# Kernel tuning notes

Measured on AMD Instinct MI355X. Metric: run time of the kernel, lower is better.

## Reference

```python
import jax, jax.numpy as jnp
import numpy as np

WS = 7; SHIFT = 3; HEADS = 4; DIM = 192; C2 = 2 * DIM; HD = C2 // HEADS
H = W = 60
PAD = (WS - H % WS) % WS          # 3
HP = H + PAD; WP = W + PAD        # 63
NW = (HP // WS) * (WP // WS)      # 81 windows
N = WS * WS                       # 49 tokens per window
MLP_H = int(4.0 * C2)             # 1536


def _rel_pos_index():
    coords = np.stack(np.meshgrid(np.arange(WS), np.arange(WS), indexing='ij'))
    cf = coords.reshape(2, -1)
    rel = (cf[:, :, None] - cf[:, None, :]).transpose(1, 2, 0)
    rel[:, :, 0] += WS - 1
    rel[:, :, 1] += WS - 1
    rel[:, :, 0] *= 2 * WS - 1
    return rel.sum(-1)  # (N, N) into table of size (2*WS-1)^2


def _attn_mask():
    img = np.zeros((HP, WP))
    cnt = 0
    for hs in (slice(0, -WS), slice(-WS, -SHIFT), slice(-SHIFT, None)):
        for ws_ in (slice(0, -WS), slice(-WS, -SHIFT), slice(-SHIFT, None)):
            img[hs, ws_] = cnt; cnt += 1
    mw = img.reshape(HP // WS, WS, WP // WS, WS).transpose(0, 2, 1, 3).reshape(-1, N)
    diff = mw[:, None, :] - mw[:, :, None]
    return np.where(diff != 0, -100.0, 0.0).astype(np.float32)  # (NW, N, N)

REL_IDX = jnp.asarray(_rel_pos_index().reshape(-1))
ATTN_MASK = jnp.asarray(_attn_mask())


def layernorm(x, w, b, eps=1e-5):
    mu = jnp.mean(x, axis=-1, keepdims=True)
    var = jnp.var(x, axis=-1, keepdims=True)
    return (x - mu) * jax.lax.rsqrt(var + eps) * w + b


def setup_inputs() -> dict:
    key = jax.random.key(0)
    ks = jax.random.split(key, 16)
    s = 0.02
    return {
        'x': jax.random.normal(ks[0], (8, DIM, H, W), jnp.float32),
        'g': jax.random.normal(ks[1], (8, DIM, H, W), jnp.float32),
        'norm_w': jnp.ones((C2,), jnp.float32),
        'norm_b': jnp.zeros((C2,), jnp.float32),
        'n1_w': jnp.ones((C2,), jnp.float32),
        'n1_b': jnp.zeros((C2,), jnp.float32),
        'qkv_w': jax.random.normal(ks[2], (3 * C2, C2), jnp.float32) * s,
        'qkv_b': jnp.zeros((3 * C2,), jnp.float32),
        'proj_w': jax.random.normal(ks[3], (C2, C2), jnp.float32) * s,
        'proj_b': jnp.zeros((C2,), jnp.float32),
        'rpb': jax.random.normal(ks[4], ((2 * WS - 1) ** 2, HEADS), jnp.float32) * s,
        'n2_w': jnp.ones((C2,), jnp.float32),
        'n2_b': jnp.zeros((C2,), jnp.float32),
        'fc1_w': jax.random.normal(ks[5], (MLP_H, C2), jnp.float32) * s,
        'fc1_b': jnp.zeros((MLP_H,), jnp.float32),
        'fc2_w': jax.random.normal(ks[6], (C2, MLP_H), jnp.float32) * s,
        'fc2_b': jnp.zeros((C2,), jnp.float32),
        'conv_w': jax.random.normal(ks[7], (DIM, C2, 3, 3), jnp.float32) * s,
        'conv_b': jnp.zeros((DIM,), jnp.float32),
    }


def reference(x, g, norm_w, norm_b, n1_w, n1_b, qkv_w, qkv_b, proj_w, proj_b,
              rpb, n2_w, n2_b, fc1_w, fc1_b, fc2_w, fc2_b, conv_w, conv_b):
    B = x.shape[0]
    # concat + NCHW -> NHWC + pad to window multiple
    comb = jnp.concatenate([x, g], axis=1).transpose(0, 2, 3, 1)   # (B,H,W,2C)
    comb = jnp.pad(comb, ((0, 0), (0, PAD), (0, PAD), (0, 0)))     # (B,HP,WP,2C)
    z = layernorm(comb, norm_w, norm_b)
    # ---- Swin block ----
    shortcut = z
    zn = layernorm(z, n1_w, n1_b)
    zn = jnp.roll(zn, shift=(-SHIFT, -SHIFT), axis=(1, 2))
    # window partition -> (B*NW, N, 2C)
    w = zn.reshape(B, HP // WS, WS, WP // WS, WS, C2).transpose(0, 1, 3, 2, 4, 5)
    w = w.reshape(B * NW, N, C2)
    qkv = (w @ qkv_w.T + qkv_b).reshape(B * NW, N, 3, HEADS, HD).transpose(2, 0, 3, 1, 4)
    q, k, v = qkv[0], qkv[1], qkv[2]                               # (B*NW,H,N,HD)
    attn = jnp.einsum('bhnd,bhmd->bhnm', q, k) * (HD ** -0.5)
    bias = rpb[REL_IDX].reshape(N, N, HEADS).transpose(2, 0, 1)    # (H,N,N)
    attn = attn + bias[None]
    attn = attn.reshape(B, NW, HEADS, N, N) + ATTN_MASK[None, :, None]
    attn = jax.nn.softmax(attn.reshape(B * NW, HEADS, N, N), axis=-1)
    out = jnp.einsum('bhnm,bhmd->bhnd', attn, v).transpose(0, 2, 1, 3).reshape(B * NW, N, C2)
    out = out @ proj_w.T + proj_b
    # window reverse + unshift
    out = out.reshape(B, HP // WS, WP // WS, WS, WS, C2).transpose(0, 1, 3, 2, 4, 5)
    out = out.reshape(B, HP, WP, C2)
    out = jnp.roll(out, shift=(SHIFT, SHIFT), axis=(1, 2))
    z = shortcut + out
    h = layernorm(z, n2_w, n2_b)
    h = jax.nn.gelu(h @ fc1_w.T + fc1_b, approximate=False)
    z = z + (h @ fc2_w.T + fc2_b)
    # crop, NHWC -> NCHW, 3x3 reduce conv, residual
    z = z[:, :H, :W, :].transpose(0, 3, 1, 2)                      # (B,2C,H,W)
    red = jax.lax.conv_general_dilated(
        z, conv_w, window_strides=(1, 1), padding=((1, 1), (1, 1)),
        dimension_numbers=('NCHW', 'OIHW', 'NCHW')) + conv_b[None, :, None, None]
    return red + x
```

## Files before the change

### kernel.cpp

```cpp
#include <hip/hip_runtime.h>
#include <cstddef>
#include <cstdint>

#define HEADS   4
#define C2c     384
#define HPc     63
#define WPc     63
#define NWc     81
#define BATCH   8
#define TOKP    (BATCH*HPc*WPc)
#define TOKC    (BATCH*60*60)
#define MLPH    1536
#define TPB     3969
#define CONVK   3456
#define CONVN   192

typedef __attribute__((ext_vector_type(8))) short short8;
typedef __attribute__((ext_vector_type(4))) float f32x4;
typedef unsigned short u16;

__device__ __forceinline__ u16 f2bf(float f) {
  unsigned u = __float_as_uint(f);
  u += 0x7fff + ((u >> 16) & 1);
  return (u16)(u >> 16);
}
__device__ __forceinline__ float bf2f(u16 b) { return __uint_as_float((unsigned)b << 16); }

#define GLOAD16(gp, lp) __builtin_amdgcn_global_load_lds( \
    (const __attribute__((address_space(1))) unsigned*)(gp), \
    (__attribute__((address_space(3))) unsigned*)(lp), 16, 0, 0)

__device__ __forceinline__ float2 block_reduce_384(float v, float* red) {
  __syncthreads();
  float s = v, q = v * v;
  #pragma unroll
  for (int o = 32; o > 0; o >>= 1) {
    s += __shfl_down(s, o);
    q += __shfl_down(q, o);
  }
  int w = threadIdx.x >> 6;
  if ((threadIdx.x & 63) == 0) { red[2*w] = s; red[2*w+1] = q; }
  __syncthreads();
  float ts = red[0]+red[2]+red[4]+red[6]+red[8]+red[10];
  float tq = red[1]+red[3]+red[5]+red[7]+red[9]+red[11];
  return make_float2(ts, tq);
}

__global__ __launch_bounds__(384)
void k1a_kernel(const float* __restrict__ x, const float* __restrict__ g,
                const float* __restrict__ nw, const float* __restrict__ nb,
                const float* __restrict__ n1w, const float* __restrict__ n1b,
                float* __restrict__ musig, u16* __restrict__ wbuf)
{
  __shared__ float red[12];
  int t = blockIdx.x;
  int b = t / (HPc*WPc);
  int rem = t - b*(HPc*WPc);
  int i = rem / WPc, j = rem - (rem / WPc)*WPc;
  int c = threadIdx.x;

  float v = 0.f;
  if (i < 60 && j < 60) {
    if (c < 192) v = x[(((size_t)b*192 + c)*60 + i)*60 + j];
    else         v = g[(((size_t)b*192 + (c-192))*60 + i)*60 + j];
  }
  float2 ss = block_reduce_384(v, red);
  float mu  = ss.x * (1.f/384.f);
  float var = ss.y * (1.f/384.f) - mu*mu;
  float rs  = rsqrtf(var + 1e-5f);
  if (c == 0) { musig[2*t] = mu; musig[2*t+1] = rs; }
  float zi  = (v - mu) * rs * nw[c] + nb[c];
  float2 s2 = block_reduce_384(zi, red);
  float mu2  = s2.x * (1.f/384.f);
  float var2 = s2.y * (1.f/384.f) - mu2*mu2;
  float zn = (zi - mu2) * rsqrtf(var2 + 1e-5f) * n1w[c] + n1b[c];
  int ai = i - 3; if (ai < 0) ai += HPc;
  int aj = j - 3; if (aj < 0) aj += WPc;
  int win = (ai/7)*9 + (aj/7);
  int tok = (ai%7)*7 + (aj%7);
  wbuf[(((size_t)b*NWc + win)*49 + tok)*C2c + c] = f2bf(zn);
}

__global__ __launch_bounds__(384)
void k1b_kernel(const float* __restrict__ x, const float* __restrict__ g,
                const float* __restrict__ nw, const float* __restrict__ nb,
                const float* __restrict__ musig, float* __restrict__ z)
{
  int tc = blockIdx.x;
  int b = tc / 3600;
  int rem = tc - b*3600;
  int i = rem / 60, j = rem - (rem/60)*60;
  int t = b*(HPc*WPc) + i*WPc + j;
  int c = threadIdx.x;
  float v;
  if (c < 192) v = x[(((size_t)b*192 + c)*60 + i)*60 + j];
  else         v = g[(((size_t)b*192 + (c-192))*60 + i)*60 + j];
  float mu = musig[2*t], rs = musig[2*t+1];
  z[(size_t)tc*C2c + c] = (v - mu) * rs * nw[c] + nb[c];
}

__global__ __launch_bounds__(384)
void ln2_kernel(const float* __restrict__ z, const float* __restrict__ nw,
                const float* __restrict__ nb, u16* __restrict__ out)
{
  __shared__ float red[12];
  int tc = blockIdx.x;
  int c = threadIdx.x;
  float v = z[(size_t)tc*C2c + c];
  float2 ss = block_reduce_384(v, red);
  float mu  = ss.x * (1.f/384.f);
  float var = ss.y * (1.f/384.f) - mu*mu;
  out[(size_t)tc*C2c + c] = f2bf((v - mu) * rsqrtf(var + 1e-5f) * nw[c] + nb[c]);
}

__global__ __launch_bounds__(256)
void f2bf_kernel(const float* __restrict__ in, u16* __restrict__ out, int n4)
{
  int t = blockIdx.x*256 + threadIdx.x;
  if (t >= n4) return;
  float4 v = ((const float4*)in)[t];
  ushort4 o;
  o.x = f2bf(v.x); o.y = f2bf(v.y); o.z = f2bf(v.z); o.w = f2bf(v.w);
  ((ushort4*)out)[t] = o;
}

__global__ void split_convw(const float* __restrict__ cw, u16* __restrict__ hi, u16* __restrict__ lo)
{
  int t = blockIdx.x*blockDim.x + threadIdx.x;
  if (t >= CONVN*CONVK) return;
  int oc = t / CONVK, k = t - oc*CONVK;
  int p = k / 384, c = k - p*384;
  float v = cw[((size_t)oc*384 + c)*9 + p];
  u16 h = f2bf(v);
  hi[t] = h;
  lo[t] = f2bf(v - bf2f(h));
}

template<int EPI>
__global__ __launch_bounds__(256)
void mfma_gemm(const u16* __restrict__ A, const u16* __restrict__ B,
               const float* __restrict__ bias, u16* __restrict__ Cb, float* __restrict__ zbuf,
               int M, int N, int K, int ldb, int addbias)
{
  __shared__ u16 As [128*64];
  __shared__ u16 Bs [128*64];
  int tid = threadIdx.x;
  int lane = tid & 63, w = tid >> 6;
  int wr = w >> 1, wc = w & 1;
  int m0 = blockIdx.y * 128, n0 = blockIdx.x * 128;
  int srow = lane >> 3, sslot = (lane & 7) ^ srow;

  f32x4 acc[4][4];
  #pragma unroll
  for (int i = 0; i < 4; ++i)
    #pragma unroll
    for (int j = 0; j < 4; ++j) acc[i][j] = (f32x4){0.f,0.f,0.f,0.f};

  char* AsB = (char*)As; char* BsB = (char*)Bs;
  int r15 = lane & 15, kq = lane >> 4;

  for (int k0 = 0; k0 < K; k0 += 64) {
    #pragma unroll
    for (int i = 0; i < 4; ++i) {
      int rblk = w*4 + i;
      int ar = m0 + rblk*8 + srow; if (ar >= M) ar = M - 1;
      int br = n0 + rblk*8 + srow;
      GLOAD16(A + (size_t)ar*K   + k0 + sslot*8, AsB + rblk*1024);
      GLOAD16(B + (size_t)br*ldb + k0 + sslot*8, BsB + rblk*1024);
    }
    __syncthreads();
    #pragma unroll
    for (int ks = 0; ks < 2; ++ks) {
      int slog = ks*4 + kq;
      short8 af[4], bf[4];
      #pragma unroll
      for (int mi = 0; mi < 4; ++mi) {
        int row = wr*64 + mi*16 + r15;
        af[mi] = *(const short8*)(AsB + row*128 + ((slog ^ (row&7))<<4));
      }
      #pragma unroll
      for (int ni = 0; ni < 4; ++ni) {
        int row = wc*64 + ni*16 + r15;
        bf[ni] = *(const short8*)(BsB + row*128 + ((slog ^ (row&7))<<4));
      }
      #pragma unroll
      for (int mi = 0; mi < 4; ++mi)
        #pragma unroll
        for (int ni = 0; ni < 4; ++ni)
          acc[mi][ni] = __builtin_amdgcn_mfma_f32_16x16x32_bf16(af[mi], bf[ni], acc[mi][ni], 0, 0, 0);
    }
    __syncthreads();
  }

  int fq = lane >> 4, fr = lane & 15;
  #pragma unroll
  for (int mi = 0; mi < 4; ++mi) {
    #pragma unroll
    for (int j = 0; j < 4; ++j) {
      int m = m0 + wr*64 + mi*16 + fq*4 + j;
      if (m >= M) continue;
      int zrow = 0; bool zok = true;
      if (EPI == 1) {
        int b = m / TPB;
        int rem = m - b*TPB;
        int win = rem / 49, tok = rem - (rem/49)*49;
        int wh = win/9, ww = win - (win/9)*9;
        int th = tok/7, tw = tok - (tok/7)*7;
        int oi = wh*7 + th + 3; if (oi >= HPc) oi -= HPc;
        int oj = ww*7 + tw + 3; if (oj >= WPc) oj -= WPc;
        zok = (oi < 60 && oj < 60);
        zrow = (b*60 + oi)*60 + oj;
      }
      #pragma unroll
      for (int ni = 0; ni < 4; ++ni) {
        int n = n0 + wc*64 + ni*16 + fr;
        float val = acc[mi][ni][j];
        if (EPI == 0) {
          Cb[(size_t)m*N + n] = f2bf(val + bias[n]);
        } else if (EPI == 1) {
          if (zok) zbuf[(size_t)zrow*C2c + n] += val + bias[n];
        } else if (EPI == 2) {
          float vv = val + bias[n];
          float ge = 0.5f*vv*(1.f + erff(vv*0.70710678118654752f));
          Cb[(size_t)m*N + n] = f2bf(ge);
        } else {
          float vv = val + (addbias ? bias[n] : 0.f);
          zbuf[(size_t)m*C2c + n] += vv;
        }
      }
    }
  }
}

__global__ __launch_bounds__(256)
void mfma_conv(const u16* __restrict__ Y, const u16* __restrict__ Bh, const u16* __restrict__ Bl,
               const float* __restrict__ cb, const float* __restrict__ xres, float* __restrict__ outp)
{
  __shared__ u16 As [128*64];
  __shared__ u16 Bsh[64*64];
  __shared__ u16 Bsl[64*64];
  int tid = threadIdx.x;
  int lane = tid & 63, w = tid >> 6;
  int wr = w >> 1, wc = w & 1;
  int m0 = blockIdx.y * 128, n0 = blockIdx.x * 64;
  int srow = lane >> 3, sslot = (lane & 7) ^ srow;

  f32x4 acc[4][2];
  #pragma unroll
  for (int i = 0; i < 4; ++i)
    #pragma unroll
    for (int j = 0; j < 2; ++j) acc[i][j] = (f32x4){0.f,0.f,0.f,0.f};

  int rowA[4], pbA[4], ohA[4], owA[4];
  #pragma unroll
  for (int i = 0; i < 4; ++i) {
    int idx = i*256 + tid;
    rowA[i] = idx >> 3;
    int pix = m0 + rowA[i];
    int pb = pix / 3600;
    int prem = pix - pb*3600;
    pbA[i] = pb; ohA[i] = prem / 60; owA[i] = prem - (prem/60)*60;
  }

  char* AsB = (char*)As; char* BhB = (char*)Bsh; char* BlB = (char*)Bsl;
  int r15 = lane & 15, kq = lane >> 4;

  for (int k0 = 0; k0 < CONVK; k0 += 64) {
    int p  = k0 / 384;
    int c0 = k0 - p*384;
    int dh = p/3 - 1, dw = (p - (p/3)*3) - 1;
    #pragma unroll
    for (int i = 0; i < 2; ++i) {
      int rblk = w*2 + i;
      int br = n0 + rblk*8 + srow;
      GLOAD16(Bh + (size_t)br*CONVK + k0 + sslot*8, BhB + rblk*1024);
      GLOAD16(Bl + (size_t)br*CONVK + k0 + sslot*8, BlB + rblk*1024);
    }
    #pragma unroll
    for (int i = 0; i < 4; ++i) {
      int idx = i*256 + tid;
      int row = rowA[i], slot = idx & 7;
      int ih = ohA[i] + dh, iw = owA[i] + dw;
      int4 v = {0,0,0,0};
      if ((unsigned)ih < 60u && (unsigned)iw < 60u)
        v = *(const int4*)(Y + (size_t)(pbA[i]*3600 + ih*60 + iw)*C2c + c0 + slot*8);
      *(int4*)(AsB + row*128 + ((slot ^ (row&7))<<4)) = v;
    }
    __syncthreads();
    #pragma unroll
    for (int ks = 0; ks < 2; ++ks) {
      int slog = ks*4 + kq;
      short8 af[4], bh[2], bl[2];
      #pragma unroll
      for (int mi = 0; mi < 4; ++mi) {
        int row = wr*64 + mi*16 + r15;
        af[mi] = *(const short8*)(AsB + row*128 + ((slog ^ (row&7))<<4));
      }
      #pragma unroll
      for (int ni = 0; ni < 2; ++ni) {
        int row = wc*32 + ni*16 + r15;
        int off = row*128 + ((slog ^ (row&7))<<4);
        bh[ni] = *(const short8*)(BhB + off);
        bl[ni] = *(const short8*)(BlB + off);
      }
      #pragma unroll
      for (int mi = 0; mi < 4; ++mi)
        #pragma unroll
        for (int ni = 0; ni < 2; ++ni) {
          acc[mi][ni] = __builtin_amdgcn_mfma_f32_16x16x32_bf16(af[mi], bh[ni], acc[mi][ni], 0, 0, 0);
          acc[mi][ni] = __builtin_amdgcn_mfma_f32_16x16x32_bf16(af[mi], bl[ni], acc[mi][ni], 0, 0, 0);
        }
    }
    __syncthreads();
  }

  int fq = lane >> 4, fr = lane & 15;
  #pragma unroll
  for (int mi = 0; mi < 4; ++mi) {
    #pragma unroll
    for (int j = 0; j < 4; ++j) {
      int m = m0 + wr*64 + mi*16 + fq*4 + j;
      int pb = m / 3600;
      int rem = m - pb*3600;
      int oh = rem / 60, ow = rem - (rem/60)*60;
      #pragma unroll
      for (int ni = 0; ni < 2; ++ni) {
        int oc = n0 + wc*32 + ni*16 + fr;
        size_t oi = ((size_t)pb*192 + oc)*3600 + oh*60 + ow;
        outp[oi] = acc[mi][ni][j] + cb[oc] + xres[oi];
      }
    }
  }
}

#define QS_STRIDE 100
#define VS_STRIDE 104
#define SS_STRIDE 53

__global__ __launch_bounds__(256)
void attn_kernel(const u16* __restrict__ qkv, const float* __restrict__ rpb,
                 u16* __restrict__ out)
{
  __shared__ float qs[52*QS_STRIDE];
  __shared__ float ks[52*QS_STRIDE];
  __shared__ float S[52*SS_STRIDE];
  int blk = blockIdx.x;
  int h   = blk & 3;
  int bw  = blk >> 2;
  int win = bw % NWc;
  const u16* base = qkv + (size_t)bw*49*1152;
  int tid = threadIdx.x;

  for (int t2 = tid; t2 < 588; t2 += 256) {
    int r = t2 / 12, dq = t2 - (t2/12)*12;
    short8 qv = *(const short8*)(base + r*1152 +       h*96 + dq*8);
    short8 kv = *(const short8*)(base + r*1152 + 384 + h*96 + dq*8);
    #pragma unroll
    for (int e = 0; e < 8; ++e) {
      qs[r*QS_STRIDE + dq*8 + e] = bf2f((u16)qv[e]);
      ks[r*QS_STRIDE + dq*8 + e] = bf2f((u16)kv[e]);
    }
  }
  __syncthreads();

  const float scale = 0.1020620726159657f;
  int wh = win / 9, ww = win - (win/9)*9;

  if (tid < 169) {
    int tr = tid / 13, tc = tid - (tid/13)*13;
    int r0 = tr*4, c0 = tc*4;
    float a[4][4] = {};
    for (int k0 = 0; k0 < 96; k0 += 4) {
      float4 qv[4], kv4[4];
      #pragma unroll
      for (int i = 0; i < 4; ++i) qv[i]  = *(const float4*)&qs[(r0+i)*QS_STRIDE + k0];
      #pragma unroll
      for (int j = 0; j < 4; ++j) kv4[j] = *(const float4*)&ks[(c0+j)*QS_STRIDE + k0];
      #pragma unroll
      for (int i = 0; i < 4; ++i)
        #pragma unroll
        for (int j = 0; j < 4; ++j)
          a[i][j] += qv[i].x*kv4[j].x + qv[i].y*kv4[j].y + qv[i].z*kv4[j].z + qv[i].w*kv4[j].w;
    }
    #pragma unroll
    for (int i = 0; i < 4; ++i) {
      int r = r0 + i;
      if (r < 49) {
        int r1 = r/7, c1 = r - (r/7)*7;
        int hp1 = wh*7 + r1, wp1 = ww*7 + c1;
        int g1 = (hp1 < 56 ? 0 : (hp1 < 60 ? 1 : 2))*3 + (wp1 < 56 ? 0 : (wp1 < 60 ? 1 : 2));
        #pragma unroll
        for (int j = 0; j < 4; ++j) {
          int c = c0 + j;
          if (c < 49) {
            int r2 = c/7, c2 = c - (c/7)*7;
            float s = a[i][j]*scale + rpb[((r1 - r2 + 6)*13 + (c1 - c2 + 6))*HEADS + h];
            int hp2 = wh*7 + r2, wp2 = ww*7 + c2;
            int g2 = (hp2 < 56 ? 0 : (hp2 < 60 ? 1 : 2))*3 + (wp2 < 56 ? 0 : (wp2 < 60 ? 1 : 2));
            if (g1 != g2) s -= 100.f;
            S[r*SS_STRIDE + c] = s;
          }
        }
      }
    }
  }
  __syncthreads();

  for (int t2 = tid; t2 < 588; t2 += 256) {
    int r = t2 / 12, dq = t2 - (t2/12)*12;
    short8 vv = *(const short8*)(base + r*1152 + 768 + h*96 + dq*8);
    #pragma unroll
    for (int e = 0; e < 8; ++e) ks[r*VS_STRIDE + dq*8 + e] = bf2f((u16)vv[e]);
  }
  if (tid < 49) {
    float mx = -1e30f;
    for (int c = 0; c < 49; ++c) mx = fmaxf(mx, S[tid*SS_STRIDE + c]);
    float sum = 0.f;
    for (int c = 0; c < 49; ++c) { float e = expf(S[tid*SS_STRIDE + c] - mx); S[tid*SS_STRIDE + c] = e; sum += e; }
    float inv = 1.f / sum;
    for (int c = 0; c < 49; ++c) S[tid*SS_STRIDE + c] *= inv;
  }
  __syncthreads();

  if (tid < 156) {
    int tr2 = tid / 12, tc2 = tid - (tid/12)*12;
    int r0 = tr2*4, d0 = tc2*8;
    float o[4][8] = {};
    for (int c = 0; c < 49; ++c) {
      float4 v0 = *(const float4*)&ks[c*VS_STRIDE + d0];
      float4 v1 = *(const float4*)&ks[c*VS_STRIDE + d0 + 4];
      #pragma unroll
      for (int i = 0; i < 4; ++i) {
        float sv = S[(r0+i)*SS_STRIDE + c];
        o[i][0] += sv*v0.x; o[i][1] += sv*v0.y; o[i][2] += sv*v0.z; o[i][3] += sv*v0.w;
        o[i][4] += sv*v1.x; o[i][5] += sv*v1.y; o[i][6] += sv*v1.z; o[i][7] += sv*v1.w;
      }
    }
    #pragma unroll
    for (int i = 0; i < 4; ++i) {
      int r = r0 + i;
      if (r >= 49) continue;
      ushort4 w0, w1;
      w0.x = f2bf(o[i][0]); w0.y = f2bf(o[i][1]); w0.z = f2bf(o[i][2]); w0.w = f2bf(o[i][3]);
      w1.x = f2bf(o[i][4]); w1.y = f2bf(o[i][5]); w1.z = f2bf(o[i][6]); w1.w = f2bf(o[i][7]);
      size_t ob = ((size_t)bw*49 + r)*C2c + h*96 + d0;
      *(ushort4*)&out[ob]     = w0;
      *(ushort4*)&out[ob + 4] = w1;
    }
  }
}

extern "C" void kernel_launch(void* const* d_in, const int* in_sizes, int n_in,
                              void* d_out, int out_size, void* d_ws, size_t ws_size,
                              hipStream_t stream)
{
  const float* x      = (const float*)d_in[0];
  const float* g      = (const float*)d_in[1];
  const float* norm_w = (const float*)d_in[2];
  const float* norm_b = (const float*)d_in[3];
  const float* n1_w   = (const float*)d_in[4];
  const float* n1_b   = (const float*)d_in[5];
  const float* qkv_w  = (const float*)d_in[6];
  const float* qkv_b  = (const float*)d_in[7];
  const float* proj_w = (const float*)d_in[8];
  const float* proj_b = (const float*)d_in[9];
  const float* rpb    = (const float*)d_in[10];
  const float* n2_w   = (const float*)d_in[11];
  const float* n2_b   = (const float*)d_in[12];
  const float* fc1_w  = (const float*)d_in[13];
  const float* fc1_b  = (const float*)d_in[14];
  const float* fc2_w  = (const float*)d_in[15];
  const float* fc2_b  = (const float*)d_in[16];
  const float* conv_w = (const float*)d_in[17];
  const float* conv_b = (const float*)d_in[18];
  float* outp = (float*)d_out;

  char* p = (char*)d_ws;
  u16* wbuf = (u16*)p;              p += (size_t)TOKP*C2c*2;
  char* qr  = p;                    p += (size_t)TOKP*1152*2;
  u16*   qkvb = (u16*)qr;
  float* z    = (float*)qr;
  u16*   hid  = (u16*)(qr + (size_t)TOKC*C2c*4);
  u16* qkvw = (u16*)p; p += 442368*2;
  u16* pw   = (u16*)p; p += 147456*2;
  u16* f1w  = (u16*)p; p += 589824*2;
  u16* f2w  = (u16*)p; p += 589824*2;
  u16* cvwh = (u16*)p; p += (size_t)CONVN*CONVK*2;
  u16* cvwl = (u16*)p; p += (size_t)CONVN*CONVK*2;
  float* musig = (float*)p; p += (size_t)TOKP*2*4;

  f2bf_kernel<<<(442368/4 + 255)/256, 256, 0, stream>>>(qkv_w, qkvw, 442368/4);
  f2bf_kernel<<<(147456/4 + 255)/256, 256, 0, stream>>>(proj_w, pw, 147456/4);
  f2bf_kernel<<<(589824/4 + 255)/256, 256, 0, stream>>>(fc1_w, f1w, 589824/4);
  f2bf_kernel<<<(589824/4 + 255)/256, 256, 0, stream>>>(fc2_w, f2w, 589824/4);
  split_convw<<<(CONVN*CONVK + 255)/256, 256, 0, stream>>>(conv_w, cvwh, cvwl);

  k1a_kernel<<<TOKP, 384, 0, stream>>>(x, g, norm_w, norm_b, n1_w, n1_b, musig, wbuf);

  mfma_gemm<0><<<dim3(9, 249), 256, 0, stream>>>(
      wbuf, qkvw, qkv_b, qkvb, nullptr, TOKP, 1152, 384, 384, 1);

  attn_kernel<<<BATCH*NWc*HEADS, 256, 0, stream>>>(qkvb, rpb, wbuf);

  k1b_kernel<<<TOKC, 384, 0, stream>>>(x, g, norm_w, norm_b, musig, z);

  mfma_gemm<1><<<dim3(3, 249), 256, 0, stream>>>(
      wbuf, pw, proj_b, nullptr, z, TOKP, 384, 384, 384, 1);

  ln2_kernel<<<TOKC, 384, 0, stream>>>(z, n2_w, n2_b, wbuf);

  for (int h0 = 0; h0 < MLPH; h0 += 384) {
    mfma_gemm<2><<<dim3(3, 225), 256, 0, stream>>>(
        wbuf, f1w + (size_t)h0*384, fc1_b + h0,
        hid, nullptr, TOKC, 384, 384, 384, 1);
    mfma_gemm<3><<<dim3(3, 225), 256, 0, stream>>>(
        hid, f2w + h0, fc2_b,
        nullptr, z, TOKC, 384, 384, MLPH, h0 == 0 ? 1 : 0);
  }

  f2bf_kernel<<<(TOKC*C2c/4 + 255)/256, 256, 0, stream>>>(z, wbuf, TOKC*C2c/4);

  mfma_conv<<<dim3(3, 225), 256, 0, stream>>>(wbuf, cvwh, cvwl, conv_b, x, outp);
}
```

Baseline: 872.5 us.

## Fuse MLP into full-width GEMMs, fold bf16 cast into fc2 epilogue, retile conv

Adds an XCD-aware block-index swizzle to the GEMM and conv kernels so that neighbouring tiles land on the same XCD and share L2. When the workspace is large enough, the MLP runs as one full-width fc1 GEMM plus one fc2 GEMM with K=1536, replacing the four chunked pairs that re-read and re-wrote z. A new epilogue variant writes both the fp32 residual and its bf16 copy, which removes the separate f2bf pass. The conv tile shrinks to 64 rows and the grid doubles, trading per-block reuse for more parallel blocks.

New measurement: 747.3 us. -14.4%, faster.

```diff
diff --git a/kernel.cpp b/kernel.cpp
--- a/kernel.cpp
+++ b/kernel.cpp
@@ -29,6 +29,12 @@
 #define GLOAD16(gp, lp) __builtin_amdgcn_global_load_lds( \
     (const __attribute__((address_space(1))) unsigned*)(gp), \
     (__attribute__((address_space(3))) unsigned*)(lp), 16, 0, 0)
+
+__device__ __forceinline__ int xcd_swizzle(int orig, int nwg) {
+  int q = nwg >> 3, r = nwg & 7;
+  int xcd = orig & 7, off = orig >> 3;
+  return (xcd < r ? xcd*(q+1) : r*(q+1) + (xcd - r)*q) + off;
+}
 
 __device__ __forceinline__ float2 block_reduce_384(float v, float* red) {
   __syncthreads();
@@ -147,7 +153,10 @@
   int tid = threadIdx.x;
   int lane = tid & 63, w = tid >> 6;
   int wr = w >> 1, wc = w & 1;
-  int m0 = blockIdx.y * 128, n0 = blockIdx.x * 128;
+  int nwg = gridDim.x * gridDim.y;
+  int swz = xcd_swizzle(blockIdx.y*gridDim.x + blockIdx.x, nwg);
+  int bx = swz % gridDim.x, by = swz / gridDim.x;
+  int m0 = by * 128, n0 = bx * 128;
   int srow = lane >> 3, sslot = (lane & 7) ^ srow;
 
   f32x4 acc[4][4];
@@ -223,9 +232,13 @@
           float vv = val + bias[n];
           float ge = 0.5f*vv*(1.f + erff(vv*0.70710678118654752f));
           Cb[(size_t)m*N + n] = f2bf(ge);
-        } else {
+        } else if (EPI == 3) {
           float vv = val + (addbias ? bias[n] : 0.f);
           zbuf[(size_t)m*C2c + n] += vv;
+        } else {
+          float vv = val + (addbias ? bias[n] : 0.f) + zbuf[(size_t)m*C2c + n];
+          zbuf[(size_t)m*C2c + n] = vv;
+          Cb[(size_t)m*C2c + n] = f2bf(vv);
         }
       }
     }
@@ -236,24 +249,27 @@
 void mfma_conv(const u16* __restrict__ Y, const u16* __restrict__ Bh, const u16* __restrict__ Bl,
                const float* __restrict__ cb, const float* __restrict__ xres, float* __restrict__ outp)
 {
-  __shared__ u16 As [128*64];
+  __shared__ u16 As [64*64];
   __shared__ u16 Bsh[64*64];
   __shared__ u16 Bsl[64*64];
   int tid = threadIdx.x;
   int lane = tid & 63, w = tid >> 6;
   int wr = w >> 1, wc = w & 1;
-  int m0 = blockIdx.y * 128, n0 = blockIdx.x * 64;
+  int nwg = gridDim.x * gridDim.y;
+  int swz = xcd_swizzle(blockIdx.y*gridDim.x + blockIdx.x, nwg);
+  int bx = swz % 3, by = swz / 3;
+  int m0 = by * 64, n0 = bx * 64;
   int srow = lane >> 3, sslot = (lane & 7) ^ srow;
 
-  f32x4 acc[4][2];
+  f32x4 acc[2][2];
   #pragma unroll
-  for (int i = 0; i < 4; ++i)
+  for (int i = 0; i < 2; ++i)
     #pragma unroll
     for (int j = 0; j < 2; ++j) acc[i][j] = (f32x4){0.f,0.f,0.f,0.f};
 
-  int rowA[4], pbA[4], ohA[4], owA[4];
+  int rowA[2], pbA[2], ohA[2], owA[2];
   #pragma unroll
-  for (int i = 0; i < 4; ++i) {
+  for (int i = 0; i < 2; ++i) {
     int idx = i*256 + tid;
     rowA[i] = idx >> 3;
     int pix = m0 + rowA[i];
@@ -277,7 +293,7 @@
       GLOAD16(Bl + (size_t)br*CONVK + k0 + sslot*8, BlB + rblk*1024);
     }
     #pragma unroll
-    for (int i = 0; i < 4; ++i) {
+    for (int i = 0; i < 2; ++i) {
       int idx = i*256 + tid;
       int row = rowA[i], slot = idx & 7;
       int ih = ohA[i] + dh, iw = owA[i] + dw;
@@ -290,10 +306,10 @@
     #pragma unroll
     for (int ks = 0; ks < 2; ++ks) {
       int slog = ks*4 + kq;
-      short8 af[4], bh[2], bl[2];
-      #pragma unroll
-      for (int mi = 0; mi < 4; ++mi) {
-        int row = wr*64 + mi*16 + r15;
+      short8 af[2], bh[2], bl[2];
+      #pragma unroll
+      for (int mi = 0; mi < 2; ++mi) {
+        int row = wr*32 + mi*16 + r15;
         af[mi] = *(const short8*)(AsB + row*128 + ((slog ^ (row&7))<<4));
       }
       #pragma unroll
@@ -304,7 +320,7 @@
         bl[ni] = *(const short8*)(BlB + off);
       }
       #pragma unroll
-      for (int mi = 0; mi < 4; ++mi)
+      for (int mi = 0; mi < 2; ++mi)
         #pragma unroll
         for (int ni = 0; ni < 2; ++ni) {
           acc[mi][ni] = __builtin_amdgcn_mfma_f32_16x16x32_bf16(af[mi], bh[ni], acc[mi][ni], 0, 0, 0);
@@ -316,10 +332,10 @@
 
   int fq = lane >> 4, fr = lane & 15;
   #pragma unroll
-  for (int mi = 0; mi < 4; ++mi) {
+  for (int mi = 0; mi < 2; ++mi) {
     #pragma unroll
     for (int j = 0; j < 4; ++j) {
-      int m = m0 + wr*64 + mi*16 + fq*4 + j;
+      int m = m0 + wr*32 + mi*16 + fq*4 + j;
       int pb = m / 3600;
       int rem = m - pb*3600;
       int oh = rem / 60, ow = rem - (rem/60)*60;
@@ -480,7 +496,7 @@
   char* qr  = p;                    p += (size_t)TOKP*1152*2;
   u16*   qkvb = (u16*)qr;
   float* z    = (float*)qr;
-  u16*   hid  = (u16*)(qr + (size_t)TOKC*C2c*4);
+  u16*   hid_c = (u16*)(qr + (size_t)TOKC*C2c*4);
   u16* qkvw = (u16*)p; p += 442368*2;
   u16* pw   = (u16*)p; p += 147456*2;
   u16* f1w  = (u16*)p; p += 589824*2;
@@ -488,6 +504,9 @@
   u16* cvwh = (u16*)p; p += (size_t)CONVN*CONVK*2;
   u16* cvwl = (u16*)p; p += (size_t)CONVN*CONVK*2;
   float* musig = (float*)p; p += (size_t)TOKP*2*4;
+  u16* hid_f = (u16*)p;
+  size_t need_full = (size_t)(p - (char*)d_ws) + (size_t)TOKC*MLPH*2;
+  bool full_mlp = ws_size >= need_full;
 
   f2bf_kernel<<<(442368/4 + 255)/256, 256, 0, stream>>>(qkv_w, qkvw, 442368/4);
   f2bf_kernel<<<(147456/4 + 255)/256, 256, 0, stream>>>(proj_w, pw, 147456/4);
@@ -509,16 +528,26 @@
 
   ln2_kernel<<<TOKC, 384, 0, stream>>>(z, n2_w, n2_b, wbuf);
 
-  for (int h0 = 0; h0 < MLPH; h0 += 384) {
-    mfma_gemm<2><<<dim3(3, 225), 256, 0, stream>>>(
-        wbuf, f1w + (size_t)h0*384, fc1_b + h0,
-        hid, nullptr, TOKC, 384, 384, 384, 1);
-    mfma_gemm<3><<<dim3(3, 225), 256, 0, stream>>>(
-        hid, f2w + h0, fc2_b,
-        nullptr, z, TOKC, 384, 384, MLPH, h0 == 0 ? 1 : 0);
-  }
-
-  f2bf_kernel<<<(TOKC*C2c/4 + 255)/256, 256, 0, stream>>>(z, wbuf, TOKC*C2c/4);
-
-  mfma_conv<<<dim3(3, 225), 256, 0, stream>>>(wbuf, cvwh, cvwl, conv_b, x, outp);
-}
+  if (full_mlp) {
+    mfma_gemm<2><<<dim3(12, 225), 256, 0, stream>>>(
+        wbuf, f1w, fc1_b, hid_f, nullptr, TOKC, MLPH, 384, 384, 1);
+    mfma_gemm<4><<<dim3(3, 225), 256, 0, stream>>>(
+        hid_f, f2w, fc2_b, wbuf, z, TOKC, 384, MLPH, MLPH, 1);
+  } else {
+    for (int h0 = 0; h0 < MLPH; h0 += 384) {
+      mfma_gemm<2><<<dim3(3, 225), 256, 0, stream>>>(
+          wbuf, f1w + (size_t)h0*384, fc1_b + h0,
+          hid_c, nullptr, TOKC, 384, 384, 384, 1);
+      if (h0 < MLPH - 384)
+        mfma_gemm<3><<<dim3(3, 225), 256, 0, stream>>>(
+            hid_c, f2w + h0, fc2_b,
+            nullptr, z, TOKC, 384, 384, MLPH, h0 == 0 ? 1 : 0);
+      else
+        mfma_gemm<4><<<dim3(3, 225), 256, 0, stream>>>(
+            hid_c, f2w + h0, fc2_b,
+            wbuf, z, TOKC, 384, 384, MLPH, 0);
+    }
+  }
+
+  mfma_conv<<<dim3(3, 450), 256, 0, stream>>>(wbuf, cvwh, cvwl, conv_b, x, outp);
+}
```
